# Performance work log

Hardware: AMD Instinct MI355X
Metric: run time of the kernel (lower is better)

The kernel has to match this reference:

```python
import jax, jax.numpy as jnp
import numpy as np

D = 1024
NH = 16
DH = D // NH
B = 2
N = 2048
EPS = 1e-5


def setup_inputs() -> dict:
    key = jax.random.key(0)
    ks = jax.random.split(key, 12)
    s = 0.02
    return {
        "x": jax.random.normal(ks[0], (B, N, D), jnp.float32),
        "Wq": jax.random.normal(ks[1], (D, D), jnp.float32) * s,
        "Wk": jax.random.normal(ks[2], (D, D), jnp.float32) * s,
        "Wv": jax.random.normal(ks[3], (D, D), jnp.float32) * s,
        "Wo": jax.random.normal(ks[4], (D, D), jnp.float32) * s,
        "bo": jnp.zeros((D,), jnp.float32),
        "ln1_scale": jnp.ones((D,), jnp.float32),
        "ln1_shift": jnp.zeros((D,), jnp.float32),
        "ln2_scale": jnp.ones((D,), jnp.float32),
        "ln2_shift": jnp.zeros((D,), jnp.float32),
        "W1": jax.random.normal(ks[5], (4 * D, D), jnp.float32) * s,
        "b1": jnp.zeros((4 * D,), jnp.float32),
        "W2": jax.random.normal(ks[6], (D, 4 * D), jnp.float32) * s,
        "b2": jnp.zeros((D,), jnp.float32),
    }


def _layernorm(x, scale, shift):
    mean = jnp.mean(x, axis=-1, keepdims=True)
    var = jnp.mean(jnp.square(x - mean), axis=-1, keepdims=True)  # unbiased=False
    return scale * ((x - mean) / jnp.sqrt(var + EPS)) + shift


def _gelu(x):
    c = jnp.sqrt(jnp.asarray(2.0 / jnp.pi, x.dtype))
    return 0.5 * x * (1.0 + jnp.tanh(c * (x + 0.044715 * x * x * x)))


def reference(x, Wq, Wk, Wv, Wo, bo, ln1_scale, ln1_shift, ln2_scale, ln2_shift, W1, b1, W2, b2):
    Bx, Nx, d = x.shape
    # pre-MHA LN
    h = _layernorm(x, ln1_scale, ln1_shift)
    # projections (torch Linear: y = h @ W.T), no bias for Wq/Wk/Wv
    q = (h @ Wq.T).reshape(Bx, Nx, NH, DH).transpose(0, 2, 1, 3)  # [B,nh,N,dh]
    k = (h @ Wk.T).reshape(Bx, Nx, NH, DH).transpose(0, 2, 1, 3)
    v = (h @ Wv.T).reshape(Bx, Nx, NH, DH).transpose(0, 2, 1, 3)
    s = jnp.einsum("bhnd,bhmd->bhnm", q, k)  # [B,nh,N,N]
    causal = jnp.tril(jnp.ones((Nx, Nx), bool))
    s = jnp.where(causal, s, -jnp.inf)
    p = jax.nn.softmax(s / jnp.sqrt(jnp.asarray(DH, s.dtype)), axis=-1)
    pv = jnp.einsum("bhnm,bhmd->bhnd", p, v)
    pv = pv.transpose(0, 2, 1, 3).reshape(Bx, Nx, d)
    attn = pv @ Wo.T + bo
    x = x + attn  # residual (dropout is identity, dpo=0)
    # pre-FFN LN + FFN
    h = _layernorm(x, ln2_scale, ln2_shift)
    h = _gelu(h @ W1.T + b1)
    h = h @ W2.T + b2
    return x + h
```

## Files before the change

### kernel.cpp

```cpp
#include <hip/hip_runtime.h>
#include <hip/hip_bf16.h>
#include <math.h>

#define Dmod   1024
#define NHmod  16
#define DHmod  64
#define Bmod   2
#define Nmod   2048
#define Mrows  (Bmod * Nmod)
#define FF     (4 * Dmod)
#define EPSLN  1e-5f

typedef __attribute__((ext_vector_type(8))) short bf16x8;
typedef __attribute__((ext_vector_type(4))) float f32x4;
typedef unsigned short ushort_t;
typedef unsigned int uint_t;

#define MFMA16x16x32(a, b, c) __builtin_amdgcn_mfma_f32_16x16x32_bf16((a), (b), (c), 0, 0, 0)

#define AS1 __attribute__((address_space(1)))
#define AS3 __attribute__((address_space(3)))

__device__ __forceinline__ void gload_lds16(const ushort_t* g, ushort_t* l) {
    __builtin_amdgcn_global_load_lds((const AS1 uint_t*)(const void*)g,
                                     (AS3 uint_t*)(void*)l, 16, 0, 0);
}

__device__ __forceinline__ ushort_t f2bf(float f) {
    union { float f; uint_t u; } v; v.f = f;
    uint_t r = v.u + 0x7FFFu + ((v.u >> 16) & 1u);
    return (ushort_t)(r >> 16);
}

__global__ __launch_bounds__(256) void cvt_kernel(const float* __restrict__ Wq, const float* __restrict__ Wk,
                                                  const float* __restrict__ Wv, const float* __restrict__ Wo,
                                                  const float* __restrict__ W1, const float* __restrict__ W2,
                                                  ushort_t* __restrict__ qkv, ushort_t* __restrict__ wo,
                                                  ushort_t* __restrict__ w1, ushort_t* __restrict__ w2) {
    int u = blockIdx.x * 256 + threadIdx.x;
    const float* src; ushort_t* dst; int i;
    float scale = 1.0f;
    if (u < 393216) {
        if (u < 131072)      { src = Wq; dst = qkv;           i = u; scale = 0.125f; }
        else if (u < 262144) { src = Wk; dst = qkv + 1048576; i = u - 131072; }
        else                 { src = Wv; dst = qkv + 2097152; i = u - 262144; }
    } else if (u < 524288)   { src = Wo; dst = wo; i = u - 393216; }
    else if (u < 1048576)    { src = W1; dst = w1; i = u - 524288; }
    else                     { src = W2; dst = w2; i = u - 1048576; }
    float4 a = ((const float4*)src)[2 * i];
    float4 b = ((const float4*)src)[2 * i + 1];
    uint4 o;
    o.x = (uint_t)f2bf(a.x * scale) | ((uint_t)f2bf(a.y * scale) << 16);
    o.y = (uint_t)f2bf(a.z * scale) | ((uint_t)f2bf(a.w * scale) << 16);
    o.z = (uint_t)f2bf(b.x * scale) | ((uint_t)f2bf(b.y * scale) << 16);
    o.w = (uint_t)f2bf(b.z * scale) | ((uint_t)f2bf(b.w * scale) << 16);
    ((uint4*)dst)[i] = o;
}

__global__ __launch_bounds__(256) void ln_bf_kernel(const float* __restrict__ x,
                                                    const float* __restrict__ scale,
                                                    const float* __restrict__ shift,
                                                    ushort_t* __restrict__ out) {
    int row = blockIdx.x;
    const float4* xr = (const float4*)(x + (size_t)row * Dmod);
    float4 v = xr[threadIdx.x];
    float s  = v.x + v.y + v.z + v.w;
    float s2 = v.x*v.x + v.y*v.y + v.z*v.z + v.w*v.w;

    __shared__ float rs[8], rs2[8];
    #pragma unroll
    for (int o = 32; o; o >>= 1) { s += __shfl_down(s, o); s2 += __shfl_down(s2, o); }
    int wave = threadIdx.x >> 6, lane = threadIdx.x & 63;
    if (lane == 0) { rs[wave] = s; rs2[wave] = s2; }
    __syncthreads();
    if (threadIdx.x == 0) {
        rs[0]  = rs[0] + rs[1] + rs[2] + rs[3];
        rs2[0] = rs2[0] + rs2[1] + rs2[2] + rs2[3];
    }
    __syncthreads();
    float mean = rs[0] * (1.0f / Dmod);
    float var  = rs2[0] * (1.0f / Dmod) - mean * mean;
    float rstd = rsqrtf(var + EPSLN);

    float4 sc = ((const float4*)scale)[threadIdx.x];
    float4 sh = ((const float4*)shift)[threadIdx.x];
    uint2 o;
    o.x = (uint_t)f2bf(sc.x * (v.x - mean) * rstd + sh.x) |
          ((uint_t)f2bf(sc.y * (v.y - mean) * rstd + sh.y) << 16);
    o.y = (uint_t)f2bf(sc.z * (v.z - mean) * rstd + sh.z) |
          ((uint_t)f2bf(sc.w * (v.w - mean) * rstd + sh.w) << 16);
    ((uint2*)(out + (size_t)row * Dmod))[threadIdx.x] = o;
}

__device__ __forceinline__ float gelu_f(float x) {
    const float c = 0.7978845608028654f;
    float u = c * (x + 0.044715f * x * x * x);
    return x / (1.0f + __expf(-2.0f * u));
}

template <int MODE, int BN>
__global__ __launch_bounds__(256) void bgemm(const ushort_t* __restrict__ A,
                                             const ushort_t* __restrict__ W,
                                             const float* __restrict__ bias,
                                             const float* __restrict__ resid,
                                             void* __restrict__ Cv,
                                             int M, int Nout, int K, int KS,
                                             int GN, int GM) {
    const int BSZ = BN * 32;
    const int NFR = BN / 32;
    __shared__ ushort_t As[3 * 4096];
    __shared__ ushort_t Bs[3 * BSZ];
    int tid  = threadIdx.x;
    int w    = tid >> 6, lane = tid & 63;
    int li   = lane & 15, g = lane >> 4;
    int wr   = w >> 1,  wc = w & 1;

    int xcd = blockIdx.x & 7;
    int c   = blockIdx.x >> 3;
    int RN  = GN >> 2;
    int RM  = GM >> 1;
    int rsz = RN * RM;
    int bz  = c / rsz;
    int r   = c - bz * rsz;
    int bm  = (xcd >> 2) * RM + r / RN;
    int bn  = (xcd & 3) * RN + r % RN;

    int srow = tid >> 2;
    int scol = ((tid & 3) ^ ((tid >> 3) & 3)) * 8;
    const ushort_t* Ag = A + (size_t)(bm * 128 + srow) * K + bz * KS + scol;
    const ushort_t* Wg = W + (size_t)(bn * BN  + srow) * K + bz * KS + scol;
    ushort_t* AsW = As + w * 512;
    ushort_t* BsW = Bs + w * 512;

    int rsw = ((g ^ ((li >> 1) & 3)) * 8);

    uint_t lbA = (uint_t)(uintptr_t)(&As[0]);
    uint_t lbB = (uint_t)(uintptr_t)(&Bs[0]);
    uint_t abase = lbA + (uint_t)(((wr * 64 + li) * 32 + rsw) * 2);
    uint_t bbase = lbB + (uint_t)(((wc * (BN / 2) + li) * 32 + rsw) * 2);

    f32x4 acc[4][NFR];
    #pragma unroll
    for (int i = 0; i < 4; i++)
        #pragma unroll
        for (int j = 0; j < NFR; j++) acc[i][j] = (f32x4){0.f, 0.f, 0.f, 0.f};

    const int NT = KS >> 5;

    auto stagef = [&](int bufA, int bufB, int t) {
        int k0 = t * 32;
        gload_lds16(Ag + k0,          AsW + bufA);
        gload_lds16(Ag + 64 * K + k0, AsW + bufA + 2048);
        gload_lds16(Wg + k0,          BsW + bufB);
        if (BN == 128) gload_lds16(Wg + 64 * K + k0, BsW + bufB + 2048);
    };

    stagef(0, 0, 0);
    stagef(4096, BSZ, 1);

    int curA = 0, curB = 0;
    int stgA = 8192, stgB = 2 * BSZ;

    for (int t = 0; t < NT; ++t) {
        if (t == NT - 1) { asm volatile("s_waitcnt vmcnt(0)" ::); }
        else if (BN == 128) { asm volatile("s_waitcnt vmcnt(4)" ::); }
        else { asm volatile("s_waitcnt vmcnt(3)" ::); }
        __builtin_amdgcn_s_barrier();
        __builtin_amdgcn_sched_barrier(0);
        if (t + 2 < NT) stagef(stgA, stgB, t + 2);
        __builtin_amdgcn_sched_barrier(0);
        bf16x8 af[4], bfr[NFR];
        uint_t aa = abase + (uint_t)(curA * 2);
        uint_t bb = bbase + (uint_t)(curB * 2);
        asm volatile("ds_read_b128 %0, %1"             : "=v"(af[0]) : "v"(aa));
        asm volatile("ds_read_b128 %0, %1 offset:1024" : "=v"(af[1]) : "v"(aa));
        asm volatile("ds_read_b128 %0, %1 offset:2048" : "=v"(af[2]) : "v"(aa));
        asm volatile("ds_read_b128 %0, %1 offset:3072" : "=v"(af[3]) : "v"(aa));
        asm volatile("ds_read_b128 %0, %1"             : "=v"(bfr[0]) : "v"(bb));
        asm volatile("ds_read_b128 %0, %1 offset:1024" : "=v"(bfr[1]) : "v"(bb));
        if (NFR == 4) {
            asm volatile("ds_read_b128 %0, %1 offset:2048" : "=v"(bfr[2]) : "v"(bb));
            asm volatile("ds_read_b128 %0, %1 offset:3072" : "=v"(bfr[3]) : "v"(bb));
        }
        asm volatile("s_waitcnt lgkmcnt(0)" ::);
        __builtin_amdgcn_sched_barrier(0);
        __builtin_amdgcn_s_setprio(1);
        #pragma unroll
        for (int mi = 0; mi < 4; mi++)
            #pragma unroll
            for (int ni = 0; ni < NFR; ni++)
                acc[mi][ni] = MFMA16x16x32(af[mi], bfr[ni], acc[mi][ni]);
        __builtin_amdgcn_s_setprio(0);
        curA = (curA == 8192) ? 0 : curA + 4096;
        curB = (curB == 2 * BSZ) ? 0 : curB + BSZ;
        stgA = (stgA == 8192) ? 0 : stgA + 4096;
        stgB = (stgB == 2 * BSZ) ? 0 : stgB + BSZ;
    }

    #pragma unroll
    for (int mi = 0; mi < 4; mi++) {
        #pragma unroll
        for (int ni = 0; ni < NFR; ni++) {
            int nn = bn * BN + wc * (BN / 2) + ni * 16 + li;
            #pragma unroll
            for (int r2 = 0; r2 < 4; r2++) {
                int m = bm * 128 + wr * 64 + mi * 16 + g * 4 + r2;
                float v = acc[mi][ni][r2];
                if (MODE == 1) {
                    float* C = (float*)Cv;
                    C[(size_t)m * Nout + nn] = v + bias[nn] + resid[(size_t)m * Nout + nn];
                } else if (MODE == 2) {
                    ushort_t* C = (ushort_t*)Cv;
                    C[(size_t)m * Nout + nn] = f2bf(gelu_f(v + bias[nn]));
                } else if (MODE == 3) {
                    float* C = (float*)Cv + (size_t)bz * M * Nout;
                    C[(size_t)m * Nout + nn] = v;
                } else {
                    int which = nn >> 10;
                    int col   = nn & 1023;
                    int h = col >> 6, d = col & 63;
                    int b = m >> 11,  n = m & (Nmod - 1);
                    ushort_t* C = (ushort_t*)Cv;
                    if (which == 0)
                        C[(((size_t)(b * NHmod + h)) * Nmod + n) * DHmod + d] = f2bf(v);
                    else if (which == 1)
                        C[4194304u + (((size_t)(b * NHmod + h)) * Nmod + n) * DHmod + d] = f2bf(v);
                    else
                        C[8388608u + (((size_t)(b * NHmod + h)) * DHmod + d) * Nmod + n] = f2bf(v);
                }
            }
        }
    }
}

__global__ __launch_bounds__(256) void red_ln_kernel(const float* __restrict__ p,
                                                     const float* __restrict__ x,
                                                     const float* __restrict__ bo,
                                                     const float* __restrict__ scale,
                                                     const float* __restrict__ shift,
                                                     float* __restrict__ x1,
                                                     ushort_t* __restrict__ h2) {
    int row = blockIdx.x;
    int t   = threadIdx.x;
    const size_t MD = (size_t)Mrows * Dmod;
    float4 a = ((const float4*)(p + (size_t)row * Dmod))[t];
    float4 b = ((const float4*)(p + MD + (size_t)row * Dmod))[t];
    float4 xr = ((const float4*)(x + (size_t)row * Dmod))[t];
    float4 bb = ((const float4*)bo)[t];
    float4 v;
    v.x = a.x + b.x + xr.x + bb.x;
    v.y = a.y + b.y + xr.y + bb.y;
    v.z = a.z + b.z + xr.z + bb.z;
    v.w = a.w + b.w + xr.w + bb.w;
    ((float4*)(x1 + (size_t)row * Dmod))[t] = v;

    float s  = v.x + v.y + v.z + v.w;
    float s2 = v.x*v.x + v.y*v.y + v.z*v.z + v.w*v.w;
    __shared__ float rs[8], rs2[8];
    #pragma unroll
    for (int o = 32; o; o >>= 1) { s += __shfl_down(s, o); s2 += __shfl_down(s2, o); }
    int wave = t >> 6, lane = t & 63;
    if (lane == 0) { rs[wave] = s; rs2[wave] = s2; }
    __syncthreads();
    if (t == 0) {
        rs[0]  = rs[0] + rs[1] + rs[2] + rs[3];
        rs2[0] = rs2[0] + rs2[1] + rs2[2] + rs2[3];
    }
    __syncthreads();
    float mean = rs[0] * (1.0f / Dmod);
    float var  = rs2[0] * (1.0f / Dmod) - mean * mean;
    float rstd = rsqrtf(var + EPSLN);

    float4 sc = ((const float4*)scale)[t];
    float4 sh = ((const float4*)shift)[t];
    uint2 o;
    o.x = (uint_t)f2bf(sc.x * (v.x - mean) * rstd + sh.x) |
          ((uint_t)f2bf(sc.y * (v.y - mean) * rstd + sh.y) << 16);
    o.y = (uint_t)f2bf(sc.z * (v.z - mean) * rstd + sh.z) |
          ((uint_t)f2bf(sc.w * (v.w - mean) * rstd + sh.w) << 16);
    ((uint2*)(h2 + (size_t)row * Dmod))[t] = o;
}

__global__ __launch_bounds__(256) void red_out_kernel(const float* __restrict__ p,
                                                      const float* __restrict__ x1,
                                                      const float* __restrict__ b2,
                                                      float* __restrict__ out) {
    const size_t MD4 = (size_t)Mrows * Dmod / 4;
    size_t i = (size_t)blockIdx.x * 256 + threadIdx.x;
    if (i >= MD4) return;
    float4 a = ((const float4*)p)[i];
    float4 b = ((const float4*)p)[MD4 + i];
    float4 xr = ((const float4*)x1)[i];
    float4 bb = ((const float4*)b2)[i & 255];
    float4 v;
    v.x = a.x + b.x + xr.x + bb.x;
    v.y = a.y + b.y + xr.y + bb.y;
    v.z = a.z + b.z + xr.z + bb.z;
    v.w = a.w + b.w + xr.w + bb.w;
    ((float4*)out)[i] = v;
}

__global__ __launch_bounds__(256) void fattn_kernel(const ushort_t* __restrict__ Q,
                                                    const ushort_t* __restrict__ K,
                                                    const ushort_t* __restrict__ VT,
                                                    ushort_t* __restrict__ O) {
    int bid = blockIdx.x;
    int xcd = bid & 7;
    int j   = bid >> 3;
    int bh  = xcd * 4 + (j & 3);
    int qt  = 31 - (j >> 2);
    int b   = bh >> 4, hh = bh & 15;
    int w    = threadIdx.x >> 6;
    int lane = threadIdx.x & 63;
    int li   = lane & 15;
    int g    = lane >> 4;

    __shared__ ushort_t Klds[2][4096];
    __shared__ ushort_t Vlds[2][4096];
    __shared__ ushort_t Plds[4][16][72];

    int q0 = qt * 64 + w * 16;
    int q  = q0 + li;

    const ushort_t* Qb = Q  + (size_t)bh * Nmod * DHmod;
    const ushort_t* Kb = K  + (size_t)bh * Nmod * DHmod;
    const ushort_t* Vb = VT + (size_t)bh * DHmod * Nmod;

    bf16x8 qf[2];
    #pragma unroll
    for (int c = 0; c < 2; c++)
        qf[c] = *(const bf16x8*)(Qb + (size_t)q * DHmod + c * 32 + g * 8);

    f32x4 po[4];
    #pragma unroll
    for (int mt = 0; mt < 4; mt++) po[mt] = (f32x4){0.f, 0.f, 0.f, 0.f};
    float l = 0.f;

    const int ntiles = qt + 1;

    int r_sub = lane >> 3;
    int cc    = ((lane & 7) ^ (r_sub & 7)) * 8;

    int swz  = (li & 7) * 8;
    int roff = li * 64;
    int c0k  = (g * 8) ^ swz;
    int c1k  = (32 + g * 8) ^ swz;

    auto stage = [&](int buf, int kt) {
        int k0 = kt * 64;
        #pragma unroll
        for (int i2 = 0; i2 < 2; i2++) {
            int i   = w * 2 + i2;
            int row = i * 8 + r_sub;
            gload_lds16(Kb + (size_t)(k0 + row) * DHmod + cc, &Klds[buf][i * 512]);
            gload_lds16(Vb + (size_t)row * Nmod + k0 + cc,    &Vlds[buf][i * 512]);
        }
    };

    stage(0, 0);

    for (int kt = 0; kt < ntiles; ++kt) {
        __syncthreads();
        if (kt + 1 < ntiles) stage((kt + 1) & 1, kt + 1);
        int cur = kt & 1;
        int k0  = kt * 64;

        f32x4 s[4];
        __builtin_amdgcn_s_setprio(1);
        #pragma unroll
        for (int mt = 0; mt < 4; mt++) {
            bf16x8 kf0 = *(const bf16x8*)&Klds[cur][mt * 1024 + roff + c0k];
            bf16x8 kf1 = *(const bf16x8*)&Klds[cur][mt * 1024 + roff + c1k];
            s[mt] = (f32x4){0.f, 0.f, 0.f, 0.f};
            s[mt] = MFMA16x16x32(kf0, qf[0], s[mt]);
            s[mt] = MFMA16x16x32(kf1, qf[1], s[mt]);
        }
        __builtin_amdgcn_s_setprio(0);

        if (kt == qt) {
            #pragma unroll
            for (int mt = 0; mt < 4; mt++)
                #pragma unroll
                for (int r = 0; r < 4; r++)
                    if (k0 + mt * 16 + g * 4 + r > q) s[mt][r] = -INFINITY;
        }
        float ptile = 0.f;
        #pragma unroll
        for (int mt = 0; mt < 4; mt++) {
            float p0 = __expf(s[mt][0]);
            float p1 = __expf(s[mt][1]);
            float p2 = __expf(s[mt][2]);
            float p3 = __expf(s[mt][3]);
            ptile += (p0 + p1) + (p2 + p3);
            uint2 pk;
            pk.x = (uint_t)f2bf(p0) | ((uint_t)f2bf(p1) << 16);
            pk.y = (uint_t)f2bf(p2) | ((uint_t)f2bf(p3) << 16);
            *(uint2*)&Plds[w][li][mt * 16 + g * 4] = pk;
        }
        l += ptile;

        asm volatile("" ::: "memory");

        bf16x8 pf0 = *(const bf16x8*)&Plds[w][li][g * 8];
        bf16x8 pf1 = *(const bf16x8*)&Plds[w][li][32 + g * 8];
        __builtin_amdgcn_s_setprio(1);
        #pragma unroll
        for (int mt = 0; mt < 4; mt++) {
            bf16x8 vf0 = *(const bf16x8*)&Vlds[cur][mt * 1024 + roff + c0k];
            bf16x8 vf1 = *(const bf16x8*)&Vlds[cur][mt * 1024 + roff + c1k];
            po[mt] = MFMA16x16x32(vf0, pf0, po[mt]);
            po[mt] = MFMA16x16x32(vf1, pf1, po[mt]);
        }
        __builtin_amdgcn_s_setprio(0);
        asm volatile("" ::: "memory");
    }

    l += __shfl_xor(l, 16);
    l += __shfl_xor(l, 32);
    float inv = 1.0f / l;
    ushort_t* Orow = O + ((size_t)(b * Nmod + q)) * Dmod + hh * DHmod;
    #pragma unroll
    for (int mt = 0; mt < 4; mt++) {
        uint2 pk;
        pk.x = (uint_t)f2bf(po[mt][0] * inv) | ((uint_t)f2bf(po[mt][1] * inv) << 16);
        pk.y = (uint_t)f2bf(po[mt][2] * inv) | ((uint_t)f2bf(po[mt][3] * inv) << 16);
        *(uint2*)(Orow + mt * 16 + g * 4) = pk;
    }
}

extern "C" void kernel_launch(void* const* d_in, const int* in_sizes, int n_in,
                              void* d_out, int out_size, void* d_ws, size_t ws_size,
                              hipStream_t stream) {
    const float* x    = (const float*)d_in[0];
    const float* Wq   = (const float*)d_in[1];
    const float* Wk   = (const float*)d_in[2];
    const float* Wv   = (const float*)d_in[3];
    const float* Wo   = (const float*)d_in[4];
    const float* bo   = (const float*)d_in[5];
    const float* ln1s = (const float*)d_in[6];
    const float* ln1b = (const float*)d_in[7];
    const float* ln2s = (const float*)d_in[8];
    const float* ln2b = (const float*)d_in[9];
    const float* W1   = (const float*)d_in[10];
    const float* b1   = (const float*)d_in[11];
    const float* W2   = (const float*)d_in[12];
    const float* b2   = (const float*)d_in[13];
    float* out = (float*)d_out;
    char*  wsb = (char*)d_ws;

    ushort_t* h_bf  = (ushort_t*)wsb;
    ushort_t* qb    = (ushort_t*)(wsb + (8u  << 20));
    ushort_t* kb    = qb + 4194304;
    ushort_t* vtb   = qb + 8388608;
    float*    x1    = (float*)(wsb + (32u << 20));
    ushort_t* h2_bf = (ushort_t*)(wsb + (48u << 20));
    ushort_t* g_bf  = (ushort_t*)(wsb + (56u << 20));
    ushort_t* wqkv  = (ushort_t*)(wsb + (88u << 20));
    ushort_t* wo_b  = (ushort_t*)(wsb + (94u << 20));
    ushort_t* w1_b  = (ushort_t*)(wsb + (96u << 20));
    ushort_t* w2_b  = (ushort_t*)(wsb + (104u << 20));
    ushort_t* att   = h_bf;
    float* pWo = (float*)(wsb + (56u << 20));
    float* pFd = (float*)wsb;

    cvt_kernel<<<6144, 256, 0, stream>>>(Wq, Wk, Wv, Wo, W1, W2, wqkv, wo_b, w1_b, w2_b);
    ln_bf_kernel<<<Mrows, 256, 0, stream>>>(x, ln1s, ln1b, h_bf);
    bgemm<0, 128><<<768, 256, 0, stream>>>(h_bf, wqkv, nullptr, nullptr, qb, Mrows, 3072, Dmod, Dmod, 24, 32);
    fattn_kernel<<<1024, 256, 0, stream>>>(qb, kb, vtb, att);
    bgemm<3, 64><<<1024, 256, 0, stream>>>(att, wo_b, nullptr, nullptr, pWo, Mrows, Dmod, Dmod, Dmod / 2, 16, 32);
    red_ln_kernel<<<Mrows, 256, 0, stream>>>(pWo, x, bo, ln2s, ln2b, x1, h2_bf);
    bgemm<2, 128><<<1024, 256, 0, stream>>>(h2_bf, w1_b, b1, nullptr, g_bf, Mrows, FF, Dmod, Dmod, 32, 32);
    bgemm<3, 64><<<1024, 256, 0, stream>>>(g_bf, w2_b, nullptr, nullptr, pFd, Mrows, Dmod, FF, FF / 2, 16, 32);
    red_out_kernel<<<(Mrows * Dmod / 4 + 255) / 256, 256, 0, stream>>>(pFd, x1, b2, out);
}
```

Baseline: 252.7 us.

## Add 256x256-tile 512-thread GEMM for FFN layers with bf16 split-K partials

Adds a new gemm256 kernel with 256x256 output tiles, 8 waves, a double-buffered LDS pipeline fed by direct global-to-LDS loads, and hand-scheduled ds_read and MFMA groups with priority hints. The FFN up-projection (with GELU) and down-projection now use it. The down-projection uses 4-way split-K and stores its partials as bf16 instead of fp32, and a new reduction kernel sums the four bf16 partials. The larger tiles are meant to raise operand reuse and MFMA density. In exchange, the grid shrinks to 256 blocks, and storing partials in bf16 costs some accuracy.

```diff
diff --git a/kernel.cpp b/kernel.cpp
--- a/kernel.cpp
+++ b/kernel.cpp
@@ -30,6 +30,11 @@
     union { float f; uint_t u; } v; v.f = f;
     uint_t r = v.u + 0x7FFFu + ((v.u >> 16) & 1u);
     return (ushort_t)(r >> 16);
+}
+
+__device__ __forceinline__ float bf2f(uint_t u) {
+    union { float f; uint_t u; } v; v.u = u << 16;
+    return v.f;
 }
 
 __global__ __launch_bounds__(256) void cvt_kernel(const float* __restrict__ Wq, const float* __restrict__ Wk,
@@ -96,6 +101,173 @@
     const float c = 0.7978845608028654f;
     float u = c * (x + 0.044715f * x * x * x);
     return x / (1.0f + __expf(-2.0f * u));
+}
+
+template <int MODE>
+__global__ __launch_bounds__(512, 2) void gemm256(const ushort_t* __restrict__ A,
+                                                  const ushort_t* __restrict__ W,
+                                                  const float* __restrict__ bias,
+                                                  void* __restrict__ Cv,
+                                                  int M, int Nout, int K, int KS,
+                                                  int GN, int GM) {
+    __shared__ ushort_t Ab[2 * 2 * 8192];
+    __shared__ ushort_t Bb[2 * 2 * 8192];
+    int tid = threadIdx.x;
+    int w  = tid >> 6, l = tid & 63;
+    int li = l & 15,  g = l >> 4;
+    int wm = w >> 2,  wn = w & 3;
+
+    int xcd = blockIdx.x & 7;
+    int c   = blockIdx.x >> 3;
+    int RN = GN >> 2, RM = GM >> 1;
+    int rsz = RN * RM;
+    int bz = c / rsz;
+    int r  = c - bz * rsz;
+    int bm = (xcd >> 2) * RM + r / RN;
+    int bn = (xcd & 3) * RN + r % RN;
+
+    int srow = w * 16 + (l >> 3);
+    int scol = ((l & 7) ^ (l >> 3)) * 8;
+    const ushort_t* Ag = A + (size_t)(bm * 256 + srow) * K + bz * KS + scol;
+    const ushort_t* Wg = W + (size_t)(bn * 256 + srow) * K + bz * KS + scol;
+
+    uint_t laneoff = (uint_t)(li * 128 + ((g ^ (li & 3)) << 4) + (((li >> 2) & 1) << 6));
+    uint_t aB0 = (uint_t)(uintptr_t)(&Ab[0]) + (uint_t)(wm * 16384) + laneoff;
+    uint_t bB0 = (uint_t)(uintptr_t)(&Bb[0]) + (uint_t)((wn >> 1) * 16384 + (wn & 1) * 8192) + laneoff;
+
+    f32x4 acc[8][4];
+    #pragma unroll
+    for (int i = 0; i < 8; i++)
+        #pragma unroll
+        for (int j = 0; j < 4; j++) acc[i][j] = (f32x4){0.f, 0.f, 0.f, 0.f};
+
+    const int NT = KS >> 6;
+
+    auto stage = [&](int d, int t) {
+        int k0 = t * 64;
+        #pragma unroll
+        for (int h = 0; h < 2; h++) {
+            #pragma unroll
+            for (int i = 0; i < 2; i++) {
+                gload_lds16(Ag + (size_t)(h * 128 + i * 8) * K + k0,
+                            &Ab[0] + (d * 2 + h) * 8192 + (w * 2 + i) * 512);
+                gload_lds16(Wg + (size_t)(h * 128 + i * 8) * K + k0,
+                            &Bb[0] + (d * 2 + h) * 8192 + (w * 2 + i) * 512);
+            }
+        }
+    };
+
+    stage(0, 0);
+
+    for (int t = 0; t < NT; ++t) {
+        int d = t & 1;
+        __syncthreads();
+        if (t + 1 < NT) stage(d ^ 1, t + 1);
+        __builtin_amdgcn_sched_barrier(0);
+
+        uint_t aa0 = aB0 + (uint_t)(d * 32768);
+        uint_t aa1 = aa0 ^ 64u;
+        uint_t bb0 = bB0 + (uint_t)(d * 32768);
+        uint_t bb1 = bb0 ^ 64u;
+
+        bf16x8 af0, af1, af2, af3, ag0, ag1, ag2, ag3;
+        bf16x8 b000, b010, b001, b011;
+        bf16x8 b100, b110, b101, b111;
+
+        asm volatile("ds_read_b128 %0, %1"             : "=v"(af0) : "v"(aa0));
+        asm volatile("ds_read_b128 %0, %1 offset:2048" : "=v"(af1) : "v"(aa0));
+        asm volatile("ds_read_b128 %0, %1 offset:4096" : "=v"(af2) : "v"(aa0));
+        asm volatile("ds_read_b128 %0, %1 offset:6144" : "=v"(af3) : "v"(aa0));
+        asm volatile("ds_read_b128 %0, %1"             : "=v"(ag0) : "v"(aa1));
+        asm volatile("ds_read_b128 %0, %1 offset:2048" : "=v"(ag1) : "v"(aa1));
+        asm volatile("ds_read_b128 %0, %1 offset:4096" : "=v"(ag2) : "v"(aa1));
+        asm volatile("ds_read_b128 %0, %1 offset:6144" : "=v"(ag3) : "v"(aa1));
+        asm volatile("ds_read_b128 %0, %1"             : "=v"(b000) : "v"(bb0));
+        asm volatile("ds_read_b128 %0, %1 offset:2048" : "=v"(b010) : "v"(bb0));
+        asm volatile("ds_read_b128 %0, %1"             : "=v"(b001) : "v"(bb1));
+        asm volatile("ds_read_b128 %0, %1 offset:2048" : "=v"(b011) : "v"(bb1));
+        asm volatile("s_waitcnt lgkmcnt(0)" ::);
+        __builtin_amdgcn_sched_barrier(0);
+        __builtin_amdgcn_s_setprio(1);
+        acc[0][0] = MFMA16x16x32(af0, b000, acc[0][0]); acc[0][0] = MFMA16x16x32(ag0, b001, acc[0][0]);
+        acc[1][0] = MFMA16x16x32(af1, b000, acc[1][0]); acc[1][0] = MFMA16x16x32(ag1, b001, acc[1][0]);
+        acc[2][0] = MFMA16x16x32(af2, b000, acc[2][0]); acc[2][0] = MFMA16x16x32(ag2, b001, acc[2][0]);
+        acc[3][0] = MFMA16x16x32(af3, b000, acc[3][0]); acc[3][0] = MFMA16x16x32(ag3, b001, acc[3][0]);
+        acc[0][1] = MFMA16x16x32(af0, b010, acc[0][1]); acc[0][1] = MFMA16x16x32(ag0, b011, acc[0][1]);
+        acc[1][1] = MFMA16x16x32(af1, b010, acc[1][1]); acc[1][1] = MFMA16x16x32(ag1, b011, acc[1][1]);
+        acc[2][1] = MFMA16x16x32(af2, b010, acc[2][1]); acc[2][1] = MFMA16x16x32(ag2, b011, acc[2][1]);
+        acc[3][1] = MFMA16x16x32(af3, b010, acc[3][1]); acc[3][1] = MFMA16x16x32(ag3, b011, acc[3][1]);
+        __builtin_amdgcn_s_setprio(0);
+
+        asm volatile("ds_read_b128 %0, %1 offset:4096" : "=v"(b100) : "v"(bb0));
+        asm volatile("ds_read_b128 %0, %1 offset:6144" : "=v"(b110) : "v"(bb0));
+        asm volatile("ds_read_b128 %0, %1 offset:4096" : "=v"(b101) : "v"(bb1));
+        asm volatile("ds_read_b128 %0, %1 offset:6144" : "=v"(b111) : "v"(bb1));
+        asm volatile("s_waitcnt lgkmcnt(0)" ::);
+        __builtin_amdgcn_sched_barrier(0);
+        __builtin_amdgcn_s_setprio(1);
+        acc[0][2] = MFMA16x16x32(af0, b100, acc[0][2]); acc[0][2] = MFMA16x16x32(ag0, b101, acc[0][2]);
+        acc[1][2] = MFMA16x16x32(af1, b100, acc[1][2]); acc[1][2] = MFMA16x16x32(ag1, b101, acc[1][2]);
+        acc[2][2] = MFMA16x16x32(af2, b100, acc[2][2]); acc[2][2] = MFMA16x16x32(ag2, b101, acc[2][2]);
+        acc[3][2] = MFMA16x16x32(af3, b100, acc[3][2]); acc[3][2] = MFMA16x16x32(ag3, b101, acc[3][2]);
+        acc[0][3] = MFMA16x16x32(af0, b110, acc[0][3]); acc[0][3] = MFMA16x16x32(ag0, b111, acc[0][3]);
+        acc[1][3] = MFMA16x16x32(af1, b110, acc[1][3]); acc[1][3] = MFMA16x16x32(ag1, b111, acc[1][3]);
+        acc[2][3] = MFMA16x16x32(af2, b110, acc[2][3]); acc[2][3] = MFMA16x16x32(ag2, b111, acc[2][3]);
+        acc[3][3] = MFMA16x16x32(af3, b110, acc[3][3]); acc[3][3] = MFMA16x16x32(ag3, b111, acc[3][3]);
+        __builtin_amdgcn_s_setprio(0);
+
+        asm volatile("ds_read_b128 %0, %1 offset:8192"  : "=v"(af0) : "v"(aa0));
+        asm volatile("ds_read_b128 %0, %1 offset:10240" : "=v"(af1) : "v"(aa0));
+        asm volatile("ds_read_b128 %0, %1 offset:12288" : "=v"(af2) : "v"(aa0));
+        asm volatile("ds_read_b128 %0, %1 offset:14336" : "=v"(af3) : "v"(aa0));
+        asm volatile("ds_read_b128 %0, %1 offset:8192"  : "=v"(ag0) : "v"(aa1));
+        asm volatile("ds_read_b128 %0, %1 offset:10240" : "=v"(ag1) : "v"(aa1));
+        asm volatile("ds_read_b128 %0, %1 offset:12288" : "=v"(ag2) : "v"(aa1));
+        asm volatile("ds_read_b128 %0, %1 offset:14336" : "=v"(ag3) : "v"(aa1));
+        asm volatile("s_waitcnt lgkmcnt(0)" ::);
+        __builtin_amdgcn_sched_barrier(0);
+        __builtin_amdgcn_s_setprio(1);
+        acc[4][0] = MFMA16x16x32(af0, b000, acc[4][0]); acc[4][0] = MFMA16x16x32(ag0, b001, acc[4][0]);
+        acc[5][0] = MFMA16x16x32(af1, b000, acc[5][0]); acc[5][0] = MFMA16x16x32(ag1, b001, acc[5][0]);
+        acc[6][0] = MFMA16x16x32(af2, b000, acc[6][0]); acc[6][0] = MFMA16x16x32(ag2, b001, acc[6][0]);
+        acc[7][0] = MFMA16x16x32(af3, b000, acc[7][0]); acc[7][0] = MFMA16x16x32(ag3, b001, acc[7][0]);
+        acc[4][1] = MFMA16x16x32(af0, b010, acc[4][1]); acc[4][1] = MFMA16x16x32(ag0, b011, acc[4][1]);
+        acc[5][1] = MFMA16x16x32(af1, b010, acc[5][1]); acc[5][1] = MFMA16x16x32(ag1, b011, acc[5][1]);
+        acc[6][1] = MFMA16x16x32(af2, b010, acc[6][1]); acc[6][1] = MFMA16x16x32(ag2, b011, acc[6][1]);
+        acc[7][1] = MFMA16x16x32(af3, b010, acc[7][1]); acc[7][1] = MFMA16x16x32(ag3, b011, acc[7][1]);
+        __builtin_amdgcn_s_setprio(0);
+
+        __builtin_amdgcn_s_setprio(1);
+        acc[4][2] = MFMA16x16x32(af0, b100, acc[4][2]); acc[4][2] = MFMA16x16x32(ag0, b101, acc[4][2]);
+        acc[5][2] = MFMA16x16x32(af1, b100, acc[5][2]); acc[5][2] = MFMA16x16x32(ag1, b101, acc[5][2]);
+        acc[6][2] = MFMA16x16x32(af2, b100, acc[6][2]); acc[6][2] = MFMA16x16x32(ag2, b101, acc[6][2]);
+        acc[7][2] = MFMA16x16x32(af3, b100, acc[7][2]); acc[7][2] = MFMA16x16x32(ag3, b101, acc[7][2]);
+        acc[4][3] = MFMA16x16x32(af0, b110, acc[4][3]); acc[4][3] = MFMA16x16x32(ag0, b111, acc[4][3]);
+        acc[5][3] = MFMA16x16x32(af1, b110, acc[5][3]); acc[5][3] = MFMA16x16x32(ag1, b111, acc[5][3]);
+        acc[6][3] = MFMA16x16x32(af2, b110, acc[6][3]); acc[6][3] = MFMA16x16x32(ag2, b111, acc[6][3]);
+        acc[7][3] = MFMA16x16x32(af3, b110, acc[7][3]); acc[7][3] = MFMA16x16x32(ag3, b111, acc[7][3]);
+        __builtin_amdgcn_s_setprio(0);
+    }
+
+    #pragma unroll
+    for (int fm = 0; fm < 8; fm++) {
+        #pragma unroll
+        for (int fn = 0; fn < 4; fn++) {
+            int nn = bn * 256 + wn * 64 + (fn >> 1) * 32 + (fn & 1) * 16 + li;
+            #pragma unroll
+            for (int r2 = 0; r2 < 4; r2++) {
+                int m = bm * 256 + wm * 128 + (fm >> 2) * 64 + (fm & 3) * 16 + g * 4 + r2;
+                float v = acc[fm][fn][r2];
+                if (MODE == 2) {
+                    ushort_t* C = (ushort_t*)Cv;
+                    C[(size_t)m * Nout + nn] = f2bf(gelu_f(v + bias[nn]));
+                } else {
+                    ushort_t* P = (ushort_t*)Cv + (size_t)bz * M * Nout;
+                    P[(size_t)m * Nout + nn] = f2bf(v);
+                }
+            }
+        }
+    }
 }
 
 template <int MODE, int BN>
@@ -281,22 +453,25 @@
     ((uint2*)(h2 + (size_t)row * Dmod))[t] = o;
 }
 
-__global__ __launch_bounds__(256) void red_out_kernel(const float* __restrict__ p,
-                                                      const float* __restrict__ x1,
-                                                      const float* __restrict__ b2,
-                                                      float* __restrict__ out) {
+__global__ __launch_bounds__(256) void red_out4_kernel(const ushort_t* __restrict__ p,
+                                                       const float* __restrict__ x1,
+                                                       const float* __restrict__ b2,
+                                                       float* __restrict__ out) {
     const size_t MD4 = (size_t)Mrows * Dmod / 4;
     size_t i = (size_t)blockIdx.x * 256 + threadIdx.x;
     if (i >= MD4) return;
-    float4 a = ((const float4*)p)[i];
-    float4 b = ((const float4*)p)[MD4 + i];
     float4 xr = ((const float4*)x1)[i];
     float4 bb = ((const float4*)b2)[i & 255];
     float4 v;
-    v.x = a.x + b.x + xr.x + bb.x;
-    v.y = a.y + b.y + xr.y + bb.y;
-    v.z = a.z + b.z + xr.z + bb.z;
-    v.w = a.w + b.w + xr.w + bb.w;
+    v.x = xr.x + bb.x; v.y = xr.y + bb.y; v.z = xr.z + bb.z; v.w = xr.w + bb.w;
+    #pragma unroll
+    for (int z = 0; z < 4; z++) {
+        uint2 pk = ((const uint2*)(p + (size_t)z * Mrows * Dmod))[i];
+        v.x += bf2f(pk.x & 0xffffu);
+        v.y += bf2f(pk.x >> 16);
+        v.z += bf2f(pk.y & 0xffffu);
+        v.w += bf2f(pk.y >> 16);
+    }
     ((float4*)out)[i] = v;
 }
 
@@ -460,8 +635,8 @@
     ushort_t* w1_b  = (ushort_t*)(wsb + (96u << 20));
     ushort_t* w2_b  = (ushort_t*)(wsb + (104u << 20));
     ushort_t* att   = h_bf;
-    float* pWo = (float*)(wsb + (56u << 20));
-    float* pFd = (float*)wsb;
+    float*    pWo = (float*)(wsb + (56u << 20));
+    ushort_t* pFd = (ushort_t*)wsb;
 
     cvt_kernel<<<6144, 256, 0, stream>>>(Wq, Wk, Wv, Wo, W1, W2, wqkv, wo_b, w1_b, w2_b);
     ln_bf_kernel<<<Mrows, 256, 0, stream>>>(x, ln1s, ln1b, h_bf);
@@ -469,7 +644,7 @@
     fattn_kernel<<<1024, 256, 0, stream>>>(qb, kb, vtb, att);
     bgemm<3, 64><<<1024, 256, 0, stream>>>(att, wo_b, nullptr, nullptr, pWo, Mrows, Dmod, Dmod, Dmod / 2, 16, 32);
     red_ln_kernel<<<Mrows, 256, 0, stream>>>(pWo, x, bo, ln2s, ln2b, x1, h2_bf);
-    bgemm<2, 128><<<1024, 256, 0, stream>>>(h2_bf, w1_b, b1, nullptr, g_bf, Mrows, FF, Dmod, Dmod, 32, 32);
-    bgemm<3, 64><<<1024, 256, 0, stream>>>(g_bf, w2_b, nullptr, nullptr, pFd, Mrows, Dmod, FF, FF / 2, 16, 32);
-    red_out_kernel<<<(Mrows * Dmod / 4 + 255) / 256, 256, 0, stream>>>(pFd, x1, b2, out);
-}
+    gemm256<2><<<256, 512, 0, stream>>>(h2_bf, w1_b, b1, g_bf, Mrows, FF, Dmod, Dmod, 16, 16);
+    gemm256<4><<<256, 512, 0, stream>>>(g_bf, w2_b, nullptr, pFd, Mrows, Dmod, FF, FF / 4, 4, 16);
+    red_out4_kernel<<<(Mrows * Dmod / 4 + 255) / 256, 256, 0, stream>>>(pFd, x1, b2, out);
+}
```

Result: faster. 231.6 us (-8.3%).

## Add 256x256-tile 8-wave GEMM for QKV, FFN1 and split-K FFN2

Applied to the files above, without the earlier changes.

Adds a new GEMM kernel with 256x256 output tiles, 512 threads, double-buffered LDS with swizzled direct-to-LDS loads, and a hand-scheduled MFMA sequence with barriers and priority hints. It replaces the QKV, FFN-up and FFN-down GEMMs. FFN-down now uses 4-way split-K with bf16 partials, and the reduction kernel sums four bf16 partials. Larger tiles raise operand reuse and cut global traffic, and bf16 partials halve partial-sum bandwidth, at the cost of fewer blocks per GPU and some precision loss in the split-K sum.

```diff
diff --git a/kernel.cpp b/kernel.cpp
--- a/kernel.cpp
+++ b/kernel.cpp
@@ -30,6 +30,11 @@
     union { float f; uint_t u; } v; v.f = f;
     uint_t r = v.u + 0x7FFFu + ((v.u >> 16) & 1u);
     return (ushort_t)(r >> 16);
+}
+
+__device__ __forceinline__ float bf2f(uint_t u) {
+    union { float f; uint_t u; } v; v.u = u << 16;
+    return v.f;
 }
 
 __global__ __launch_bounds__(256) void cvt_kernel(const float* __restrict__ Wq, const float* __restrict__ Wk,
@@ -98,6 +103,177 @@
     return x / (1.0f + __expf(-2.0f * u));
 }
 
+#define DSR(D, A, OFF) asm volatile("ds_read_b128 %0, %1 offset:" OFF : "=v"(D) : "v"(A))
+#define SB0 __builtin_amdgcn_sched_barrier(0)
+#define BARR __builtin_amdgcn_s_barrier()
+#define LGKM0 asm volatile("s_waitcnt lgkmcnt(0)" ::)
+
+#define MMQ0 \
+  acc[0][0]=MFMA16x16x32(a0,b0,acc[0][0]); acc[1][0]=MFMA16x16x32(a1,b0,acc[1][0]); \
+  acc[2][0]=MFMA16x16x32(a2,b0,acc[2][0]); acc[3][0]=MFMA16x16x32(a3,b0,acc[3][0]); \
+  acc[0][1]=MFMA16x16x32(a0,b1,acc[0][1]); acc[1][1]=MFMA16x16x32(a1,b1,acc[1][1]); \
+  acc[2][1]=MFMA16x16x32(a2,b1,acc[2][1]); acc[3][1]=MFMA16x16x32(a3,b1,acc[3][1]); \
+  acc[0][2]=MFMA16x16x32(a0,b2,acc[0][2]); acc[1][2]=MFMA16x16x32(a1,b2,acc[1][2]); \
+  acc[2][2]=MFMA16x16x32(a2,b2,acc[2][2]); acc[3][2]=MFMA16x16x32(a3,b2,acc[3][2]); \
+  acc[0][3]=MFMA16x16x32(a0,b3,acc[0][3]); acc[1][3]=MFMA16x16x32(a1,b3,acc[1][3]); \
+  acc[2][3]=MFMA16x16x32(a2,b3,acc[2][3]); acc[3][3]=MFMA16x16x32(a3,b3,acc[3][3]);
+#define MMQ4 \
+  acc[4][0]=MFMA16x16x32(a0,b0,acc[4][0]); acc[5][0]=MFMA16x16x32(a1,b0,acc[5][0]); \
+  acc[6][0]=MFMA16x16x32(a2,b0,acc[6][0]); acc[7][0]=MFMA16x16x32(a3,b0,acc[7][0]); \
+  acc[4][1]=MFMA16x16x32(a0,b1,acc[4][1]); acc[5][1]=MFMA16x16x32(a1,b1,acc[5][1]); \
+  acc[6][1]=MFMA16x16x32(a2,b1,acc[6][1]); acc[7][1]=MFMA16x16x32(a3,b1,acc[7][1]); \
+  acc[4][2]=MFMA16x16x32(a0,b2,acc[4][2]); acc[5][2]=MFMA16x16x32(a1,b2,acc[5][2]); \
+  acc[6][2]=MFMA16x16x32(a2,b2,acc[6][2]); acc[7][2]=MFMA16x16x32(a3,b2,acc[7][2]); \
+  acc[4][3]=MFMA16x16x32(a0,b3,acc[4][3]); acc[5][3]=MFMA16x16x32(a1,b3,acc[5][3]); \
+  acc[6][3]=MFMA16x16x32(a2,b3,acc[6][3]); acc[7][3]=MFMA16x16x32(a3,b3,acc[7][3]);
+
+template <int MODE>
+__global__ __launch_bounds__(512, 2) void gemm256(const ushort_t* __restrict__ A,
+                                                  const ushort_t* __restrict__ W,
+                                                  const float* __restrict__ bias,
+                                                  void* __restrict__ Cv,
+                                                  int M, int Nout, int K, int KS,
+                                                  int GN, int GM) {
+    __shared__ ushort_t Ab[32768];
+    __shared__ ushort_t Bb[32768];
+    int tid = threadIdx.x;
+    int w  = tid >> 6, l = tid & 63;
+    int li = l & 15,  g = l >> 4;
+    int wm = w >> 2,  wn = w & 3;
+
+    int xcd = blockIdx.x & 7;
+    int c   = blockIdx.x >> 3;
+    int RN = GN >> 2, RM = GM >> 1;
+    int rsz = RN * RM;
+    int bz = c / rsz;
+    int r  = c - bz * rsz;
+    int bm = (xcd >> 2) * RM + r / RN;
+    int bn = (xcd & 3) * RN + r % RN;
+
+    int lc   = (l & 7) ^ (l >> 3);
+    int sgr  = w * 32 + 2 * (l >> 3) + (lc >> 2);
+    int colo = (lc & 3) * 8;
+    const ushort_t* sA0 = A + (size_t)(bm * 256 + sgr) * K + bz * KS + colo;
+    const ushort_t* sA1 = sA0 + (size_t)16 * K;
+    const ushort_t* sB0 = W + (size_t)(bn * 256 + sgr) * K + bz * KS + colo;
+    const ushort_t* sB1 = sB0 + (size_t)16 * K;
+
+    uint_t chunkpos = (uint_t)(((((li & 1) << 2) + g) ^ (li >> 1)) << 4);
+    uint_t aBase = (uint_t)(uintptr_t)(&Ab[0]) + (uint_t)(wm * 8192 + (li >> 1) * 128) + chunkpos;
+    uint_t bBase = (uint_t)(uintptr_t)(&Bb[0]) + (uint_t)(wn * 4096 + (li >> 1) * 128) + chunkpos;
+
+    f32x4 acc[8][4];
+    #pragma unroll
+    for (int i = 0; i < 8; i++)
+        #pragma unroll
+        for (int j = 0; j < 4; j++) acc[i][j] = (f32x4){0.f, 0.f, 0.f, 0.f};
+
+    const int NT = KS >> 6;
+
+    {
+        ushort_t* dA = &Ab[0] + w * 1024;
+        ushort_t* dB = &Bb[0] + w * 1024;
+        gload_lds16(sA0,      dA);        gload_lds16(sA1,      dA + 512);
+        gload_lds16(sB0,      dB);        gload_lds16(sB1,      dB + 512);
+        gload_lds16(sA0 + 32, dA + 8192); gload_lds16(sA1 + 32, dA + 8192 + 512);
+        gload_lds16(sB0 + 32, dB + 8192); gload_lds16(sB1 + 32, dB + 8192 + 512);
+    }
+    asm volatile("s_waitcnt vmcnt(4)" ::);
+    SB0; BARR;
+
+    for (int t = 0; t < NT; ++t) {
+        int d = t & 1;
+        bool pf = (t + 1 < NT);
+        int kn = (t + 1) * 64;
+        uint_t aAddr = aBase + (uint_t)(d * 32768);
+        uint_t bAddr = bBase + (uint_t)(d * 32768);
+        ushort_t* dA = &Ab[0] + (d ^ 1) * 16384 + w * 1024;
+        ushort_t* dB = &Bb[0] + (d ^ 1) * 16384 + w * 1024;
+        bf16x8 a0, a1, a2, a3, b0, b1, b2, b3;
+
+        DSR(a0, aAddr, "0");    DSR(a1, aAddr, "1024");
+        DSR(a2, aAddr, "2048"); DSR(a3, aAddr, "3072");
+        DSR(b0, bAddr, "0");    DSR(b1, bAddr, "1024");
+        DSR(b2, bAddr, "2048"); DSR(b3, bAddr, "3072");
+        if (pf) { gload_lds16(sA0 + kn, dA); gload_lds16(sA1 + kn, dA + 512); }
+        SB0; BARR; LGKM0; SB0;
+        __builtin_amdgcn_s_setprio(1);
+        MMQ0
+        __builtin_amdgcn_s_setprio(0);
+        SB0; BARR;
+
+        DSR(a0, aAddr, "4096"); DSR(a1, aAddr, "5120");
+        DSR(a2, aAddr, "6144"); DSR(a3, aAddr, "7168");
+        if (pf) { gload_lds16(sB0 + kn, dB); gload_lds16(sB1 + kn, dB + 512); }
+        SB0; BARR; LGKM0; SB0;
+        __builtin_amdgcn_s_setprio(1);
+        MMQ4
+        __builtin_amdgcn_s_setprio(0);
+        if (pf) { asm volatile("s_waitcnt vmcnt(4)" ::); }
+        else    { asm volatile("s_waitcnt vmcnt(0)" ::); }
+        SB0; BARR;
+
+        DSR(a0, aAddr, "16384"); DSR(a1, aAddr, "17408");
+        DSR(a2, aAddr, "18432"); DSR(a3, aAddr, "19456");
+        DSR(b0, bAddr, "16384"); DSR(b1, bAddr, "17408");
+        DSR(b2, bAddr, "18432"); DSR(b3, bAddr, "19456");
+        if (pf) { gload_lds16(sA0 + kn + 32, dA + 8192); gload_lds16(sA1 + kn + 32, dA + 8192 + 512); }
+        SB0; BARR; LGKM0; SB0;
+        __builtin_amdgcn_s_setprio(1);
+        MMQ0
+        __builtin_amdgcn_s_setprio(0);
+        SB0; BARR;
+
+        DSR(a0, aAddr, "20480"); DSR(a1, aAddr, "21504");
+        DSR(a2, aAddr, "22528"); DSR(a3, aAddr, "23552");
+        if (pf) { gload_lds16(sB0 + kn + 32, dB + 8192); gload_lds16(sB1 + kn + 32, dB + 8192 + 512); }
+        SB0; BARR; LGKM0; SB0;
+        __builtin_amdgcn_s_setprio(1);
+        MMQ4
+        __builtin_amdgcn_s_setprio(0);
+        asm volatile("s_waitcnt vmcnt(4)" ::);
+        SB0; BARR;
+    }
+
+    #pragma unroll
+    for (int fm = 0; fm < 8; fm++) {
+        #pragma unroll
+        for (int fn = 0; fn < 4; fn++) {
+            int nn = bn * 256 + wn * 64 + fn * 16 + li;
+            int mB = bm * 256 + wm * 128 + (fm >> 2) * 64 + (fm & 3) * 16 + g * 4;
+            if (MODE == 0) {
+                int which = nn >> 10, col = nn & 1023;
+                int h = col >> 6, dd = col & 63;
+                int b = mB >> 11, n0 = mB & (Nmod - 1);
+                ushort_t* C = (ushort_t*)Cv;
+                if (which == 2) {
+                    uint2 pk;
+                    pk.x = (uint_t)f2bf(acc[fm][fn][0]) | ((uint_t)f2bf(acc[fm][fn][1]) << 16);
+                    pk.y = (uint_t)f2bf(acc[fm][fn][2]) | ((uint_t)f2bf(acc[fm][fn][3]) << 16);
+                    *(uint2*)(C + 8388608u + (((size_t)(b * NHmod + h)) * DHmod + dd) * Nmod + n0) = pk;
+                } else {
+                    #pragma unroll
+                    for (int r2 = 0; r2 < 4; r2++) {
+                        size_t idx = (size_t)which * 4194304u +
+                                     (((size_t)(b * NHmod + h)) * Nmod + n0 + r2) * DHmod + dd;
+                        C[idx] = f2bf(acc[fm][fn][r2]);
+                    }
+                }
+            } else if (MODE == 2) {
+                ushort_t* C = (ushort_t*)Cv;
+                #pragma unroll
+                for (int r2 = 0; r2 < 4; r2++)
+                    C[(size_t)(mB + r2) * Nout + nn] = f2bf(gelu_f(acc[fm][fn][r2] + bias[nn]));
+            } else {
+                ushort_t* P = (ushort_t*)Cv + (size_t)bz * M * Nout;
+                #pragma unroll
+                for (int r2 = 0; r2 < 4; r2++)
+                    P[(size_t)(mB + r2) * Nout + nn] = f2bf(acc[fm][fn][r2]);
+            }
+        }
+    }
+}
+
 template <int MODE, int BN>
 __global__ __launch_bounds__(256) void bgemm(const ushort_t* __restrict__ A,
                                              const ushort_t* __restrict__ W,
@@ -209,24 +385,9 @@
                 if (MODE == 1) {
                     float* C = (float*)Cv;
                     C[(size_t)m * Nout + nn] = v + bias[nn] + resid[(size_t)m * Nout + nn];
-                } else if (MODE == 2) {
-                    ushort_t* C = (ushort_t*)Cv;
-                    C[(size_t)m * Nout + nn] = f2bf(gelu_f(v + bias[nn]));
                 } else if (MODE == 3) {
                     float* C = (float*)Cv + (size_t)bz * M * Nout;
                     C[(size_t)m * Nout + nn] = v;
-                } else {
-                    int which = nn >> 10;
-                    int col   = nn & 1023;
-                    int h = col >> 6, d = col & 63;
-                    int b = m >> 11,  n = m & (Nmod - 1);
-                    ushort_t* C = (ushort_t*)Cv;
-                    if (which == 0)
-                        C[(((size_t)(b * NHmod + h)) * Nmod + n) * DHmod + d] = f2bf(v);
-                    else if (which == 1)
-                        C[4194304u + (((size_t)(b * NHmod + h)) * Nmod + n) * DHmod + d] = f2bf(v);
-                    else
-                        C[8388608u + (((size_t)(b * NHmod + h)) * DHmod + d) * Nmod + n] = f2bf(v);
                 }
             }
         }
@@ -281,22 +442,25 @@
     ((uint2*)(h2 + (size_t)row * Dmod))[t] = o;
 }
 
-__global__ __launch_bounds__(256) void red_out_kernel(const float* __restrict__ p,
-                                                      const float* __restrict__ x1,
-                                                      const float* __restrict__ b2,
-                                                      float* __restrict__ out) {
+__global__ __launch_bounds__(256) void red_out4_kernel(const ushort_t* __restrict__ p,
+                                                       const float* __restrict__ x1,
+                                                       const float* __restrict__ b2,
+                                                       float* __restrict__ out) {
     const size_t MD4 = (size_t)Mrows * Dmod / 4;
     size_t i = (size_t)blockIdx.x * 256 + threadIdx.x;
     if (i >= MD4) return;
-    float4 a = ((const float4*)p)[i];
-    float4 b = ((const float4*)p)[MD4 + i];
     float4 xr = ((const float4*)x1)[i];
     float4 bb = ((const float4*)b2)[i & 255];
     float4 v;
-    v.x = a.x + b.x + xr.x + bb.x;
-    v.y = a.y + b.y + xr.y + bb.y;
-    v.z = a.z + b.z + xr.z + bb.z;
-    v.w = a.w + b.w + xr.w + bb.w;
+    v.x = xr.x + bb.x; v.y = xr.y + bb.y; v.z = xr.z + bb.z; v.w = xr.w + bb.w;
+    #pragma unroll
+    for (int z = 0; z < 4; z++) {
+        uint2 pk = ((const uint2*)(p + (size_t)z * Mrows * Dmod))[i];
+        v.x += bf2f(pk.x & 0xffffu);
+        v.y += bf2f(pk.x >> 16);
+        v.z += bf2f(pk.y & 0xffffu);
+        v.w += bf2f(pk.y >> 16);
+    }
     ((float4*)out)[i] = v;
 }
 
@@ -460,16 +624,16 @@
     ushort_t* w1_b  = (ushort_t*)(wsb + (96u << 20));
     ushort_t* w2_b  = (ushort_t*)(wsb + (104u << 20));
     ushort_t* att   = h_bf;
-    float* pWo = (float*)(wsb + (56u << 20));
-    float* pFd = (float*)wsb;
+    float*    pWo = (float*)(wsb + (56u << 20));
+    ushort_t* pFd = (ushort_t*)wsb;
 
     cvt_kernel<<<6144, 256, 0, stream>>>(Wq, Wk, Wv, Wo, W1, W2, wqkv, wo_b, w1_b, w2_b);
     ln_bf_kernel<<<Mrows, 256, 0, stream>>>(x, ln1s, ln1b, h_bf);
-    bgemm<0, 128><<<768, 256, 0, stream>>>(h_bf, wqkv, nullptr, nullptr, qb, Mrows, 3072, Dmod, Dmod, 24, 32);
+    gemm256<0><<<192, 512, 0, stream>>>(h_bf, wqkv, nullptr, qb, Mrows, 3072, Dmod, Dmod, 12, 16);
     fattn_kernel<<<1024, 256, 0, stream>>>(qb, kb, vtb, att);
     bgemm<3, 64><<<1024, 256, 0, stream>>>(att, wo_b, nullptr, nullptr, pWo, Mrows, Dmod, Dmod, Dmod / 2, 16, 32);
     red_ln_kernel<<<Mrows, 256, 0, stream>>>(pWo, x, bo, ln2s, ln2b, x1, h2_bf);
-    bgemm<2, 128><<<1024, 256, 0, stream>>>(h2_bf, w1_b, b1, nullptr, g_bf, Mrows, FF, Dmod, Dmod, 32, 32);
-    bgemm<3, 64><<<1024, 256, 0, stream>>>(g_bf, w2_b, nullptr, nullptr, pFd, Mrows, Dmod, FF, FF / 2, 16, 32);
-    red_out_kernel<<<(Mrows * Dmod / 4 + 255) / 256, 256, 0, stream>>>(pFd, x1, b2, out);
-}
+    gemm256<2><<<256, 512, 0, stream>>>(h2_bf, w1_b, b1, g_bf, Mrows, FF, Dmod, Dmod, 16, 16);
+    gemm256<4><<<256, 512, 0, stream>>>(g_bf, w2_b, nullptr, pFd, Mrows, Dmod, FF, FF / 4, 4, 16);
+    red_out4_kernel<<<(Mrows * Dmod / 4 + 255) / 256, 256, 0, stream>>>(pFd, x1, b2, out);
+}
```

Result: faster. 220.6 us (-12.7%).
